# Kernel optimization log

Measured on AMD Instinct MI355X. Metric: run time of the kernel, lower is better.

## Reference

```python
import jax, jax.numpy as jnp
import numpy as np

B, L, D = 2, 2048, 1024
H = 16
HD = D // H
TOP_FRAC = 0.2


def setup_inputs() -> dict:
    key = jax.random.key(0)
    ks = jax.random.split(key, 9)
    s = 1.0 / np.sqrt(D)
    return {
        "x": jax.random.normal(ks[0], (B, L, D), dtype=jnp.float32),
        "Wq": jax.random.normal(ks[1], (D, D), dtype=jnp.float32) * s,
        "bq": jnp.zeros((D,), jnp.float32),
        "Wk": jax.random.normal(ks[2], (D, D), dtype=jnp.float32) * s,
        "bk": jnp.zeros((D,), jnp.float32),
        "Wv": jax.random.normal(ks[3], (D, D), dtype=jnp.float32) * s,
        "bv": jnp.zeros((D,), jnp.float32),
        "Wo": jax.random.normal(ks[4], (D, D), dtype=jnp.float32) * s,
        "bo": jnp.zeros((D,), jnp.float32),
    }


def reference(x, Wq, bq, Wk, bk, Wv, bv, Wo, bo):
    b, l, d = x.shape
    scale = HD ** (-0.5)
    k_top = max(1, int(l * TOP_FRAC))

    def split_heads(t):  # [B,L,D] -> [B,H,L,HD]
        return t.reshape(b, l, H, HD).transpose(0, 2, 1, 3)

    q = split_heads(x @ Wq.T + bq)
    k = split_heads(x @ Wk.T + bk)
    v = split_heads(x @ Wv.T + bv)

    # select top-k queries per (batch, head) by squared L2 norm
    q_norm = jnp.sum(q * q, axis=-1)              # [B,H,L]
    _, topk_idx = jax.lax.top_k(q_norm, k_top)    # [B,H,k_top]
    bi = jnp.arange(b)[:, None, None]
    hi = jnp.arange(H)[None, :, None]
    mask = jnp.zeros((b, H, l), dtype=bool).at[bi, hi, topk_idx].set(True)
    q = q * mask[..., None]                       # zero non-selected queries

    scores = jnp.einsum("bhqd,bhkd->bhqk", q, k) * scale
    probs = jax.nn.softmax(scores, axis=-1)       # zero rows -> uniform 1/L
    out = jnp.einsum("bhqk,bhkd->bhqd", probs, v)
    out = out.transpose(0, 2, 1, 3).reshape(b, l, d)
    return out @ Wo.T + bo
```

## Files before the change

kernel.cpp:

```cpp
#include <hip/hip_runtime.h>
#include <hip/hip_bf16.h>
#include <math.h>

typedef __bf16 bf16_t;
typedef __bf16 bf16x8 __attribute__((ext_vector_type(8)));
typedef __bf16 bf16x4 __attribute__((ext_vector_type(4)));
typedef float  f32x4  __attribute__((ext_vector_type(4)));

#define L_DIM 2048
#define D_DIM 1024
#define H_DIM 16
#define M_DIM 4096
#define KTOP 409
#define SLOTS 512
#define SLOTS_IO 448
#define KSPLIT 8
#define KCHUNK 256
#define HSZ (L_DIM * 64)

__device__ __forceinline__ void split2(float a, bf16_t& h, bf16_t& l) {
  h = (bf16_t)a;
  l = (bf16_t)(a - (float)h);
}

__device__ __forceinline__ void gld16(const bf16_t* g, bf16_t* l) {
  __builtin_amdgcn_global_load_lds(
      (const __attribute__((address_space(1))) void*)g,
      (__attribute__((address_space(3))) void*)l, 16, 0, 0);
}

#define STAGE_TILE128(src, dst)                                               \
  {                                                                           \
    const int seg0 = wave * 2;                                                \
    const int r0 = seg0 * 16 + (lane >> 2);                                   \
    const int c0 = (((lane & 3) ^ ((lane >> 2) & 3))) * 8;                    \
    gld16((src) + (size_t)r0 * D_DIM + c0, (dst) + seg0 * 512);               \
    gld16((src) + (size_t)(r0 + 16) * D_DIM + c0, (dst) + (seg0 + 1) * 512);  \
  }

#define STAGE_TILE64(src, dst)                                                \
  {                                                                           \
    const int r0 = wave * 16 + (lane >> 2);                                   \
    const int c0 = (((lane & 3) ^ ((lane >> 2) & 3))) * 8;                    \
    gld16((src) + (size_t)r0 * D_DIM + c0, (dst) + wave * 512);               \
  }

#define FRAG(buf, ROW) \
  (*reinterpret_cast<const bf16x8*>(&(buf)[(ROW) * 32 + (quad ^ (lm & 3)) * 8]))

__global__ __launch_bounds__(256) void prep_kernel(
    const float* __restrict__ x,  const float* __restrict__ Wq,
    const float* __restrict__ Wk, const float* __restrict__ Wv,
    const float* __restrict__ Wo,
    bf16_t* __restrict__ xhi, bf16_t* __restrict__ xlo,
    bf16_t* __restrict__ Wqhi, bf16_t* __restrict__ Wqlo,
    bf16_t* __restrict__ Wkb,  bf16_t* __restrict__ Wvb,
    bf16_t* __restrict__ Wob,  float* __restrict__ Vmeanf)
{
  const int XV = (M_DIM * D_DIM) / 4;
  const int WV = (D_DIM * D_DIM) / 4;
  const int TOT = XV + 4 * WV + 512;
  for (int i = blockIdx.x * 256 + threadIdx.x; i < TOT; i += gridDim.x * 256) {
    if (i < XV) {
      f32x4 v = ((const f32x4*)x)[i];
      bf16x4 h, l;
      #pragma unroll
      for (int j = 0; j < 4; ++j) { bf16_t hh, ll; split2(v[j], hh, ll); h[j] = hh; l[j] = ll; }
      ((bf16x4*)xhi)[i] = h;
      ((bf16x4*)xlo)[i] = l;
    } else if (i < XV + WV) {
      int j0 = i - XV;
      f32x4 v = ((const f32x4*)Wq)[j0];
      bf16x4 h, l;
      #pragma unroll
      for (int j = 0; j < 4; ++j) { bf16_t hh, ll; split2(v[j], hh, ll); h[j] = hh; l[j] = ll; }
      ((bf16x4*)Wqhi)[j0] = h;
      ((bf16x4*)Wqlo)[j0] = l;
    } else if (i < XV + 2 * WV) {
      int j0 = i - XV - WV;
      f32x4 v = ((const f32x4*)Wk)[j0];
      bf16x4 h;
      #pragma unroll
      for (int j = 0; j < 4; ++j) h[j] = (bf16_t)v[j];
      ((bf16x4*)Wkb)[j0] = h;
    } else if (i < XV + 3 * WV) {
      int j0 = i - XV - 2 * WV;
      f32x4 v = ((const f32x4*)Wv)[j0];
      bf16x4 h;
      #pragma unroll
      for (int j = 0; j < 4; ++j) h[j] = (bf16_t)v[j];
      ((bf16x4*)Wvb)[j0] = h;
    } else if (i < XV + 4 * WV) {
      int j0 = i - XV - 3 * WV;
      f32x4 v = ((const f32x4*)Wo)[j0];
      bf16x4 h;
      #pragma unroll
      for (int j = 0; j < 4; ++j) h[j] = (bf16_t)v[j];
      ((bf16x4*)Wob)[j0] = h;
    } else {
      int j0 = i - XV - 4 * WV;
      f32x4 zz = {0.f, 0.f, 0.f, 0.f};
      ((f32x4*)Vmeanf)[j0] = zz;
    }
  }
}

__global__ __launch_bounds__(256, 3) void gemm_qkv(
    const bf16_t* __restrict__ xhi, const bf16_t* __restrict__ xlo,
    const bf16_t* __restrict__ Wqhi, const bf16_t* __restrict__ Wqlo,
    const bf16_t* __restrict__ Wkb, const bf16_t* __restrict__ Wvb,
    const float* __restrict__ bq, const float* __restrict__ bk, const float* __restrict__ bv,
    bf16_t* __restrict__ Qhi, bf16_t* __restrict__ Khi, bf16_t* __restrict__ VThi,
    float* __restrict__ norms, float* __restrict__ Vmeanf)
{
  const int bx = blockIdx.x;
  const int z  = bx % 3;
  const int id = bx / 3;
  const int n0   = (id & 7) * 128;
  const int row0 = (id >> 3) * 128;

  __shared__ __align__(16) bf16_t sm[2][3][4096];

  const int tid  = threadIdx.x;
  const int lane = tid & 63;
  const int wave = tid >> 6;
  const int wr = wave >> 1, wc = wave & 1;
  const int lm = lane & 15, quad = lane >> 4;

  const f32x4 vzero = {0.f, 0.f, 0.f, 0.f};
  f32x4 acc[4][4];
  #pragma unroll
  for (int mi = 0; mi < 4; ++mi)
    #pragma unroll
    for (int ni = 0; ni < 4; ++ni) acc[mi][ni] = vzero;

  if (z == 0) {
#define STAGE_A(k0, b) do {                                                  \
      STAGE_TILE128(xhi  + (size_t)row0 * D_DIM + (k0), sm[b][0]);           \
      STAGE_TILE128(Wqhi + (size_t)n0   * D_DIM + (k0), sm[b][1]);           \
      STAGE_TILE128(Wqlo + (size_t)n0   * D_DIM + (k0), sm[b][2]);           \
    } while (0)
#define STAGE_B(k0, b) do {                                                  \
      STAGE_TILE128(xlo  + (size_t)row0 * D_DIM + (k0), sm[b][0]);           \
      STAGE_TILE128(Wqhi + (size_t)n0   * D_DIM + (k0), sm[b][1]);           \
    } while (0)

    STAGE_A(0, 0);
    __syncthreads();
    int cur = 0;
    for (int k0 = 0; k0 < D_DIM; k0 += 32) {
      if (k0 + 32 < D_DIM) STAGE_A(k0 + 32, cur ^ 1);
      else                 STAGE_B(0, cur ^ 1);
      bf16x8 af[4], bh0[4], bl0[4];
      #pragma unroll
      for (int mi = 0; mi < 4; ++mi)
        af[mi] = FRAG(sm[cur][0], wr * 64 + mi * 16 + lm);
      #pragma unroll
      for (int ni = 0; ni < 4; ++ni) {
        bh0[ni] = FRAG(sm[cur][1], wc * 64 + ni * 16 + lm);
        bl0[ni] = FRAG(sm[cur][2], wc * 64 + ni * 16 + lm);
      }
      #pragma unroll
      for (int mi = 0; mi < 4; ++mi)
        #pragma unroll
        for (int ni = 0; ni < 4; ++ni) {
          acc[mi][ni] = __builtin_amdgcn_mfma_f32_16x16x32_bf16(af[mi], bh0[ni], acc[mi][ni], 0, 0, 0);
          acc[mi][ni] = __builtin_amdgcn_mfma_f32_16x16x32_bf16(af[mi], bl0[ni], acc[mi][ni], 0, 0, 0);
        }
      __syncthreads();
      cur ^= 1;
    }
    for (int k0 = 0; k0 < D_DIM; k0 += 32) {
      if (k0 + 32 < D_DIM) STAGE_B(k0 + 32, cur ^ 1);
      bf16x8 af[4], bh0[4];
      #pragma unroll
      for (int mi = 0; mi < 4; ++mi)
        af[mi] = FRAG(sm[cur][0], wr * 64 + mi * 16 + lm);
      #pragma unroll
      for (int ni = 0; ni < 4; ++ni)
        bh0[ni] = FRAG(sm[cur][1], wc * 64 + ni * 16 + lm);
      #pragma unroll
      for (int mi = 0; mi < 4; ++mi)
        #pragma unroll
        for (int ni = 0; ni < 4; ++ni)
          acc[mi][ni] = __builtin_amdgcn_mfma_f32_16x16x32_bf16(af[mi], bh0[ni], acc[mi][ni], 0, 0, 0);
      __syncthreads();
      cur ^= 1;
    }

    float bvv[4];
    #pragma unroll
    for (int ni = 0; ni < 4; ++ni) bvv[ni] = bq[n0 + wc * 64 + ni * 16 + lm];
    #pragma unroll
    for (int mi = 0; mi < 4; ++mi)
      #pragma unroll
      for (int ni = 0; ni < 4; ++ni)
        #pragma unroll
        for (int r = 0; r < 4; ++r) acc[mi][ni][r] += bvv[ni];

    const int h = (n0 + wc * 64) >> 6;
    #pragma unroll
    for (int mi = 0; mi < 4; ++mi)
      #pragma unroll
      for (int r = 0; r < 4; ++r) {
        float s = 0.f;
        #pragma unroll
        for (int ni = 0; ni < 4; ++ni) { float v = acc[mi][ni][r]; s += v * v; }
        s += __shfl_xor(s, 1); s += __shfl_xor(s, 2);
        s += __shfl_xor(s, 4); s += __shfl_xor(s, 8);
        if (lm == 0) {
          int row = row0 + wr * 64 + mi * 16 + quad * 4 + r;
          int bb = row >> 11, ll = row & (L_DIM - 1);
          norms[(bb * H_DIM + h) * L_DIM + ll] = s;
        }
      }

    #pragma unroll
    for (int mi = 0; mi < 4; ++mi)
      #pragma unroll
      for (int r = 0; r < 4; ++r) {
        int row = row0 + wr * 64 + mi * 16 + quad * 4 + r;
        #pragma unroll
        for (int ni = 0; ni < 4; ++ni)
          Qhi[(size_t)row * D_DIM + n0 + wc * 64 + ni * 16 + lm] = (bf16_t)acc[mi][ni][r];
      }
  } else {
    const bf16_t* W = (z == 1) ? Wkb : Wvb;
#define STAGE_L(k0, b) do {                                                  \
      STAGE_TILE128(xhi + (size_t)row0 * D_DIM + (k0), sm[b][0]);            \
      STAGE_TILE128(W   + (size_t)n0   * D_DIM + (k0), sm[b][1]);            \
    } while (0)

    STAGE_L(0, 0);
    __syncthreads();
    int cur = 0;
    for (int k0 = 0; k0 < D_DIM; k0 += 32) {
      if (k0 + 32 < D_DIM) STAGE_L(k0 + 32, cur ^ 1);
      bf16x8 af[4], bfr[4];
      #pragma unroll
      for (int mi = 0; mi < 4; ++mi)
        af[mi] = FRAG(sm[cur][0], wr * 64 + mi * 16 + lm);
      #pragma unroll
      for (int ni = 0; ni < 4; ++ni)
        bfr[ni] = FRAG(sm[cur][1], wc * 64 + ni * 16 + lm);
      #pragma unroll
      for (int mi = 0; mi < 4; ++mi)
        #pragma unroll
        for (int ni = 0; ni < 4; ++ni)
          acc[mi][ni] = __builtin_amdgcn_mfma_f32_16x16x32_bf16(af[mi], bfr[ni], acc[mi][ni], 0, 0, 0);
      __syncthreads();
      cur ^= 1;
    }

    const float* bias = (z == 1) ? bk : bv;
    float bvv[4];
    #pragma unroll
    for (int ni = 0; ni < 4; ++ni) bvv[ni] = bias[n0 + wc * 64 + ni * 16 + lm];
    #pragma unroll
    for (int mi = 0; mi < 4; ++mi)
      #pragma unroll
      for (int ni = 0; ni < 4; ++ni)
        #pragma unroll
        for (int r = 0; r < 4; ++r) acc[mi][ni][r] += bvv[ni];

    const int hh = (n0 + wc * 64) >> 6;
    if (z == 1) {
      #pragma unroll
      for (int mi = 0; mi < 4; ++mi)
        #pragma unroll
        for (int r = 0; r < 4; ++r) {
          int row = row0 + wr * 64 + mi * 16 + quad * 4 + r;
          int bb = row >> 11, ll = row & (L_DIM - 1);
          size_t base = (size_t)(bb * H_DIM + hh) * HSZ + (size_t)ll * 64;
          #pragma unroll
          for (int ni = 0; ni < 4; ++ni)
            Khi[base + ni * 16 + lm] = (bf16_t)acc[mi][ni][r];
        }
    } else {
      #pragma unroll
      for (int mi = 0; mi < 4; ++mi) {
        int rbase = row0 + wr * 64 + mi * 16 + quad * 4;
        int bb = rbase >> 11, l0 = rbase & (L_DIM - 1);
        int kbv = l0 >> 5, kin = l0 & 31;
        size_t hb = (size_t)(bb * H_DIM + hh) * HSZ;
        #pragma unroll
        for (int ni = 0; ni < 4; ++ni) {
          int d = ni * 16 + lm;
          bf16x4 wv;
          #pragma unroll
          for (int r = 0; r < 4; ++r) wv[r] = (bf16_t)acc[mi][ni][r];
          *reinterpret_cast<bf16x4*>(&VThi[hb + (size_t)(kbv * 64 + d) * 32 + kin]) = wv;
        }
      }
      const int bb = row0 >> 11;
      float ps[4];
      #pragma unroll
      for (int ni = 0; ni < 4; ++ni) {
        float s = 0.f;
        #pragma unroll
        for (int mi = 0; mi < 4; ++mi)
          #pragma unroll
          for (int r = 0; r < 4; ++r) s += acc[mi][ni][r];
        ps[ni] = s;
      }
      #pragma unroll
      for (int ni = 0; ni < 4; ++ni) {
        ps[ni] += __shfl_xor(ps[ni], 16);
        ps[ni] += __shfl_xor(ps[ni], 32);
      }
      if (quad == 0) {
        #pragma unroll
        for (int ni = 0; ni < 4; ++ni)
          atomicAdd(&Vmeanf[(bb * H_DIM + hh) * 64 + ni * 16 + lm], ps[ni]);
      }
    }
  }
}

__global__ __launch_bounds__(256) void gemm_out(
    const bf16_t* __restrict__ Ahi, const bf16_t* __restrict__ Wob,
    const float* __restrict__ bias, float* __restrict__ C)
{
  const int n0   = blockIdx.x * 128;
  const int row0 = blockIdx.y * 64;

  __shared__ __align__(16) bf16_t sm[2][6144];

  const int tid  = threadIdx.x;
  const int lane = tid & 63;
  const int wave = tid >> 6;
  const int wr = wave >> 1, wc = wave & 1;
  const int lm = lane & 15, quad = lane >> 4;

  const f32x4 vzero = {0.f, 0.f, 0.f, 0.f};
  f32x4 acc[2][4];
  #pragma unroll
  for (int mi = 0; mi < 2; ++mi)
    #pragma unroll
    for (int ni = 0; ni < 4; ++ni) acc[mi][ni] = vzero;

#define STAGE_O(k0, b) do {                                                  \
    STAGE_TILE64(Ahi + (size_t)row0 * D_DIM + (k0), sm[b]);                  \
    STAGE_TILE128(Wob + (size_t)n0 * D_DIM + (k0), sm[b] + 2048);            \
  } while (0)

  STAGE_O(0, 0);
  __syncthreads();
  int cur = 0;
  for (int k0 = 0; k0 < D_DIM; k0 += 32) {
    if (k0 + 32 < D_DIM) STAGE_O(k0 + 32, cur ^ 1);
    bf16x8 af[2], bfr[4];
    #pragma unroll
    for (int mi = 0; mi < 2; ++mi)
      af[mi] = FRAG(sm[cur], wr * 32 + mi * 16 + lm);
    #pragma unroll
    for (int ni = 0; ni < 4; ++ni)
      bfr[ni] = FRAG(sm[cur] + 2048, wc * 64 + ni * 16 + lm);
    #pragma unroll
    for (int mi = 0; mi < 2; ++mi)
      #pragma unroll
      for (int ni = 0; ni < 4; ++ni)
        acc[mi][ni] = __builtin_amdgcn_mfma_f32_16x16x32_bf16(af[mi], bfr[ni], acc[mi][ni], 0, 0, 0);
    __syncthreads();
    cur ^= 1;
  }

  float bvv[4];
  #pragma unroll
  for (int ni = 0; ni < 4; ++ni) bvv[ni] = bias[n0 + wc * 64 + ni * 16 + lm];
  #pragma unroll
  for (int mi = 0; mi < 2; ++mi)
    #pragma unroll
    for (int r = 0; r < 4; ++r) {
      int row = row0 + wr * 32 + mi * 16 + quad * 4 + r;
      #pragma unroll
      for (int ni = 0; ni < 4; ++ni)
        C[(size_t)row * D_DIM + n0 + wc * 64 + ni * 16 + lm] = acc[mi][ni][r] + bvv[ni];
    }
}

__global__ __launch_bounds__(1024) void topk_kernel(
    const float* __restrict__ norms, int* __restrict__ sel,
    int* __restrict__ rowmap)
{
  const int bh = blockIdx.x;
  const int t  = threadIdx.x;
  const int w  = t >> 6;
  const int lane = t & 63;

  __shared__ int bins[256];
  __shared__ unsigned int sh_pfx;
  __shared__ int sh_r;
  __shared__ int cnt0[16], cnt1[16], ecnt0[16], ecnt1[16];

  const unsigned int k0 = __float_as_uint(norms[bh * L_DIM + t]);
  const unsigned int k1 = __float_as_uint(norms[bh * L_DIM + t + 1024]);

  rowmap[bh * L_DIM + t] = -1;
  rowmap[bh * L_DIM + t + 1024] = -1;

  unsigned int pfx = 0;
  int r = KTOP;
  #pragma unroll
  for (int p = 0; p < 4; ++p) {
    const int sh = 24 - 8 * p;
    if (t < 256) bins[t] = 0;
    __syncthreads();
    const bool q0 = (p == 0) || ((k0 >> (sh + 8)) == pfx);
    const bool q1 = (p == 0) || ((k1 >> (sh + 8)) == pfx);
    if (q0) atomicAdd(&bins[(k0 >> sh) & 255], 1);
    if (q1) atomicAdd(&bins[(k1 >> sh) & 255], 1);
    __syncthreads();
    if (w == 0) {
      const int b0 = bins[lane * 4 + 0];
      const int b1 = bins[lane * 4 + 1];
      const int b2 = bins[lane * 4 + 2];
      const int b3 = bins[lane * 4 + 3];
      int sfx = b0 + b1 + b2 + b3;
      #pragma unroll
      for (int off = 1; off < 64; off <<= 1) {
        int other = __shfl_down(sfx, off);
        if (lane + off < 64) sfx += other;
      }
      int nsfx = __shfl_down(sfx, 1);
      if (lane == 63) nsfx = 0;
      if (sfx >= r && nsfx < r) {
        int cum = nsfx, B, rn;
        if (cum + b3 >= r)      { B = lane * 4 + 3; rn = r - cum; }
        else { cum += b3;
          if (cum + b2 >= r)    { B = lane * 4 + 2; rn = r - cum; }
          else { cum += b2;
            if (cum + b1 >= r)  { B = lane * 4 + 1; rn = r - cum; }
            else { cum += b1;     B = lane * 4 + 0; rn = r - cum; }
          }
        }
        sh_pfx = (pfx << 8) | (unsigned int)B;
        sh_r = rn;
      }
    }
    __syncthreads();
    pfx = sh_pfx;
    r = sh_r;
    __syncthreads();
  }
  const unsigned int T = pfx;

  const bool gt0 = (k0 > T), gt1 = (k1 > T);
  const bool eq0 = (k0 == T), eq1 = (k1 == T);
  const unsigned long long mlt = (lane == 63) ? 0x7fffffffffffffffull
                                              : ((1ull << lane) - 1ull);
  const unsigned long long bg0 = __ballot(gt0);
  const unsigned long long bg1 = __ballot(gt1);
  const unsigned long long be0 = __ballot(eq0);
  const unsigned long long be1 = __ballot(eq1);
  if (lane == 0) {
    cnt0[w]  = __popcll(bg0);
    cnt1[w]  = __popcll(bg1);
    ecnt0[w] = __popcll(be0);
    ecnt1[w] = __popcll(be1);
  }
  __syncthreads();
  int og0 = 0, og1 = 0, oe0 = 0, oe1 = 0;
  int tg0 = 0, tg1 = 0, te0 = 0;
  #pragma unroll
  for (int i = 0; i < 16; ++i) {
    if (i < w) { og0 += cnt0[i]; og1 += cnt1[i]; oe0 += ecnt0[i]; oe1 += ecnt1[i]; }
    tg0 += cnt0[i]; tg1 += cnt1[i]; te0 += ecnt0[i];
  }
  const int G = tg0 + tg1;
  const int take = KTOP - G;
  const int base = bh * SLOTS;

  if (gt0) {
    int slot = og0 + __popcll(bg0 & mlt);
    sel[base + slot] = t;
    rowmap[bh * L_DIM + t] = slot;
  }
  if (gt1) {
    int slot = tg0 + og1 + __popcll(bg1 & mlt);
    sel[base + slot] = t + 1024;
    rowmap[bh * L_DIM + t + 1024] = slot;
  }
  if (eq0) {
    int rk = oe0 + __popcll(be0 & mlt);
    if (rk < take) {
      sel[base + G + rk] = t;
      rowmap[bh * L_DIM + t] = G + rk;
    }
  }
  if (eq1) {
    int rk = te0 + oe1 + __popcll(be1 & mlt);
    if (rk < take) {
      sel[base + G + rk] = t + 1024;
      rowmap[bh * L_DIM + t + 1024] = G + rk;
    }
  }
  if (t < SLOTS - KTOP) sel[base + KTOP + t] = -1;
}

__global__ __launch_bounds__(256) void attn_kernel(
    const bf16_t* __restrict__ Qhi,
    const bf16_t* __restrict__ Khi,
    const bf16_t* __restrict__ VThi,
    const int* __restrict__ sel,
    float* __restrict__ Ol, bf16_t* __restrict__ Oo)
{
  const int bx = blockIdx.x;
  const int xl = bx & 7;
  const int rest = bx >> 3;
  const int qc = rest & 3;
  const int gh = rest >> 2;
  const int g  = gh * 8 + xl;
  const int bh = g & 31;
  const int ks = g >> 5;
  const int b = bh >> 4, h = bh & 15;
  const int wave = threadIdx.x >> 6;
  const int lane = threadIdx.x & 63;
  const int lm = lane & 15, quad = lane >> 4;

  __shared__ __align__(16) bf16_t sPh[2][2][4][16][40];

  const int qbase = qc * 128 + wave * 32;
  bf16x8 qa[2][2];
  #pragma unroll
  for (int qt = 0; qt < 2; ++qt) {
    int qi = sel[bh * SLOTS + qbase + qt * 16 + lm];
    size_t qo = ((size_t)(b * L_DIM + (qi >= 0 ? qi : 0))) * D_DIM + h * 64;
    qa[qt][0] = *reinterpret_cast<const bf16x8*>(&Qhi[qo + quad * 8]);
    qa[qt][1] = *reinterpret_cast<const bf16x8*>(&Qhi[qo + 32 + quad * 8]);
  }

  const f32x4 vzero = {0.f, 0.f, 0.f, 0.f};
  float l_l[2][4];
  f32x4 o[2][4];
  #pragma unroll
  for (int qt = 0; qt < 2; ++qt)
    #pragma unroll
    for (int ni = 0; ni < 4; ++ni) { o[qt][ni] = vzero; l_l[qt][ni] = 0.f; }

  const float scale = 0.125f;
  const size_t khead = (size_t)(b * H_DIM + h) * HSZ;
  const int key0 = ks * KCHUNK;

  #pragma unroll 2
  for (int kt = 0; kt < KCHUNK; kt += 32) {
    const int PB = (kt >> 5) & 1;
    size_t kr0 = khead + (size_t)(key0 + kt + lm) * 64;
    size_t kr1 = khead + (size_t)(key0 + kt + 16 + lm) * 64;
    bf16x8 kb0 = *reinterpret_cast<const bf16x8*>(&Khi[kr0 + quad * 8]);
    bf16x8 kb1 = *reinterpret_cast<const bf16x8*>(&Khi[kr0 + 32 + quad * 8]);
    bf16x8 kb2 = *reinterpret_cast<const bf16x8*>(&Khi[kr1 + quad * 8]);
    bf16x8 kb3 = *reinterpret_cast<const bf16x8*>(&Khi[kr1 + 32 + quad * 8]);
    const int kbv = (key0 + kt) >> 5;
    bf16x8 vbh[4];
    #pragma unroll
    for (int ni = 0; ni < 4; ++ni) {
      size_t vo = khead + (size_t)(kbv * 64 + ni * 16 + lm) * 32 + quad * 8;
      vbh[ni] = *reinterpret_cast<const bf16x8*>(&VThi[vo]);
    }
    #pragma unroll
    for (int qt = 0; qt < 2; ++qt) {
      f32x4 s0 = vzero, s1 = vzero;
      s0 = __builtin_amdgcn_mfma_f32_16x16x32_bf16(qa[qt][0], kb0, s0, 0, 0, 0);
      s0 = __builtin_amdgcn_mfma_f32_16x16x32_bf16(qa[qt][1], kb1, s0, 0, 0, 0);
      s1 = __builtin_amdgcn_mfma_f32_16x16x32_bf16(qa[qt][0], kb2, s1, 0, 0, 0);
      s1 = __builtin_amdgcn_mfma_f32_16x16x32_bf16(qa[qt][1], kb3, s1, 0, 0, 0);
      #pragma unroll
      for (int r = 0; r < 4; ++r) {
        float p0 = __expf(s0[r] * scale);
        float p1 = __expf(s1[r] * scale);
        l_l[qt][r] += p0 + p1;
        sPh[PB][qt][wave][quad * 4 + r][lm]      = (bf16_t)p0;
        sPh[PB][qt][wave][quad * 4 + r][16 + lm] = (bf16_t)p1;
      }
      bf16x8 pah = *reinterpret_cast<const bf16x8*>(&sPh[PB][qt][wave][lm][quad * 8]);
      #pragma unroll
      for (int ni = 0; ni < 4; ++ni)
        o[qt][ni] = __builtin_amdgcn_mfma_f32_16x16x32_bf16(pah, vbh[ni], o[qt][ni], 0, 0, 0);
    }
  }

  #pragma unroll
  for (int qt = 0; qt < 2; ++qt)
    #pragma unroll
    for (int r = 0; r < 4; ++r) {
      l_l[qt][r] += __shfl_xor(l_l[qt][r], 1);
      l_l[qt][r] += __shfl_xor(l_l[qt][r], 2);
      l_l[qt][r] += __shfl_xor(l_l[qt][r], 4);
      l_l[qt][r] += __shfl_xor(l_l[qt][r], 8);
    }

  #pragma unroll
  for (int qt = 0; qt < 2; ++qt)
    #pragma unroll
    for (int r = 0; r < 4; ++r) {
      int slot = qbase + qt * 16 + quad * 4 + r;
      int s2 = sel[bh * SLOTS + slot];
      if (s2 >= 0) {
        size_t gs = (size_t)(bh * SLOTS_IO + slot) * KSPLIT + ks;
        if (lm == 0) Ol[gs] = l_l[qt][r];
        #pragma unroll
        for (int ni = 0; ni < 4; ++ni)
          Oo[gs * 64 + ni * 16 + lm] = (bf16_t)o[qt][ni][r];
      }
    }
}

__global__ __launch_bounds__(256) void fill_kernel(
    const float* __restrict__ Ol, const bf16_t* __restrict__ Oo,
    const int* __restrict__ rowmap, const float* __restrict__ Vmeanf,
    bf16_t* __restrict__ AOhi)
{
  const int bh = blockIdx.x;
  const int b = bh >> 4, h = bh & 15;
  const int t = threadIdx.x;
  const int lane = t & 63;
  const int w = t >> 6;

  __shared__ __align__(16) bf16_t smh[64];
  if (t < 64)
    smh[t] = (bf16_t)(Vmeanf[(b * H_DIM + h) * 64 + t] * (1.0f / (float)L_DIM));
  __syncthreads();

  const int rbase = blockIdx.y * 64 + w * 16;
  int flag = -1;
  if (lane < 16) flag = rowmap[bh * L_DIM + rbase + lane];

  for (int j = 0; j < 16; ++j) {
    const int s = __shfl(flag, j);
    const int row = rbase + j;
    bf16_t outv;
    if (s < 0) {
      outv = smh[lane];
    } else {
      size_t gs = (size_t)(bh * SLOTS_IO + s) * KSPLIT;
      float L = 0.f, ov = 0.f;
      #pragma unroll
      for (int sp = 0; sp < KSPLIT; ++sp) {
        L  += Ol[gs + sp];
        ov += (float)Oo[(gs + sp) * 64 + lane];
      }
      outv = (bf16_t)(ov / L);
    }
    AOhi[((size_t)(b * L_DIM + row)) * D_DIM + h * 64 + lane] = outv;
  }
}

extern "C" void kernel_launch(void* const* d_in, const int* in_sizes, int n_in,
                              void* d_out, int out_size, void* d_ws, size_t ws_size,
                              hipStream_t stream) {
  const float* x  = (const float*)d_in[0];
  const float* Wq = (const float*)d_in[1];
  const float* bq = (const float*)d_in[2];
  const float* Wk = (const float*)d_in[3];
  const float* bk = (const float*)d_in[4];
  const float* Wv = (const float*)d_in[5];
  const float* bv = (const float*)d_in[6];
  const float* Wo = (const float*)d_in[7];
  const float* bo = (const float*)d_in[8];
  float* out = (float*)d_out;

  const size_t MB = 1u << 20;
  char* ws = (char*)d_ws;
  bf16_t* Qhi  = (bf16_t*)(ws);
  bf16_t* VThi = (bf16_t*)(ws + 8 * MB);
  bf16_t* xhi  = (bf16_t*)(ws + 16 * MB);
  bf16_t* xlo  = (bf16_t*)(ws + 24 * MB);
  bf16_t* Oo   = (bf16_t*)(ws + 16 * MB);
  int*    rowmap = (int*)(ws + 31 * MB);
  bf16_t* Wqhi = (bf16_t*)(ws + 32 * MB);
  bf16_t* Wqlo = (bf16_t*)(ws + 34 * MB);
  bf16_t* Wkb  = (bf16_t*)(ws + 36 * MB);
  bf16_t* Wvb  = (bf16_t*)(ws + 38 * MB);
  bf16_t* Wob  = (bf16_t*)(ws + 40 * MB);
  float*  norms = (float*)(ws + 42 * MB);
  int*    sel   = (int*)(ws + 42 * MB + (256u << 10));
  float*  Ol    = (float*)(ws + 42 * MB + (320u << 10));
  float*  Vmeanf = (float*)(ws + 42 * MB + (832u << 10));
  bf16_t* AOhi = Qhi;
  bf16_t* Khi = (bf16_t*)d_out;

  dim3 blk(256);
  prep_kernel<<<dim3(2048), blk, 0, stream>>>(x, Wq, Wk, Wv, Wo,
                                              xhi, xlo, Wqhi, Wqlo, Wkb, Wvb, Wob,
                                              Vmeanf);
  gemm_qkv<<<dim3(768), blk, 0, stream>>>(xhi, xlo, Wqhi, Wqlo, Wkb, Wvb,
                                          bq, bk, bv, Qhi, Khi, VThi, norms, Vmeanf);
  topk_kernel<<<dim3(32), dim3(1024), 0, stream>>>(norms, sel, rowmap);
  attn_kernel<<<dim3(32 * 4 * KSPLIT), blk, 0, stream>>>(Qhi, Khi, VThi, sel, Ol, Oo);
  fill_kernel<<<dim3(32, 32), blk, 0, stream>>>(Ol, Oo, rowmap, Vmeanf, AOhi);
  gemm_out<<<dim3(8, 64), blk, 0, stream>>>(AOhi, Wob, bo, out);
}
```

Measured before the change: 214.0 us.

## Stage K/V tiles through double-buffered LDS with XOR swizzle in attention

```diff
diff --git a/kernel.cpp b/kernel.cpp
--- a/kernel.cpp
+++ b/kernel.cpp
@@ -518,6 +518,8 @@
   const int lane = threadIdx.x & 63;
   const int lm = lane & 15, quad = lane >> 4;
 
+  __shared__ __align__(16) bf16_t sK[2][2048];
+  __shared__ __align__(16) bf16_t sV[2][2048];
   __shared__ __align__(16) bf16_t sPh[2][2][4][16][40];
 
   const int qbase = qc * 128 + wave * 32;
@@ -542,21 +544,34 @@
   const size_t khead = (size_t)(b * H_DIM + h) * HSZ;
   const int key0 = ks * KCHUNK;
 
+#define ATTN_STAGE(KT, bsel) do {                                             \
+    const int krow = wave * 8 + (lane >> 3);                                  \
+    const int kslot = (lane & 7) ^ ((lane >> 3) & 7);                         \
+    gld16(&Khi[khead + (size_t)(key0 + (KT) + krow) * 64 + kslot * 8],        \
+          sK[bsel] + wave * 512);                                             \
+    const int vrow = wave * 16 + (lane >> 2);                                 \
+    const int vslot = (lane & 3) ^ ((lane >> 2) & 3);                         \
+    const size_t vbase = khead + (size_t)((key0 + (KT)) >> 5) * 2048;         \
+    gld16(&VThi[vbase + vrow * 32 + vslot * 8], sV[bsel] + wave * 512);       \
+  } while (0)
+
+  ATTN_STAGE(0, 0);
+  __syncthreads();
+  int cur = 0;
   #pragma unroll 2
   for (int kt = 0; kt < KCHUNK; kt += 32) {
+    if (kt + 32 < KCHUNK) ATTN_STAGE(kt + 32, cur ^ 1);
     const int PB = (kt >> 5) & 1;
-    size_t kr0 = khead + (size_t)(key0 + kt + lm) * 64;
-    size_t kr1 = khead + (size_t)(key0 + kt + 16 + lm) * 64;
-    bf16x8 kb0 = *reinterpret_cast<const bf16x8*>(&Khi[kr0 + quad * 8]);
-    bf16x8 kb1 = *reinterpret_cast<const bf16x8*>(&Khi[kr0 + 32 + quad * 8]);
-    bf16x8 kb2 = *reinterpret_cast<const bf16x8*>(&Khi[kr1 + quad * 8]);
-    bf16x8 kb3 = *reinterpret_cast<const bf16x8*>(&Khi[kr1 + 32 + quad * 8]);
-    const int kbv = (key0 + kt) >> 5;
+    const int kx = lm & 7;
+    bf16x8 kb0 = *reinterpret_cast<const bf16x8*>(&sK[cur][lm * 64 + ((quad) ^ kx) * 8]);
+    bf16x8 kb1 = *reinterpret_cast<const bf16x8*>(&sK[cur][lm * 64 + ((quad + 4) ^ kx) * 8]);
+    bf16x8 kb2 = *reinterpret_cast<const bf16x8*>(&sK[cur][(16 + lm) * 64 + ((quad) ^ kx) * 8]);
+    bf16x8 kb3 = *reinterpret_cast<const bf16x8*>(&sK[cur][(16 + lm) * 64 + ((quad + 4) ^ kx) * 8]);
     bf16x8 vbh[4];
     #pragma unroll
     for (int ni = 0; ni < 4; ++ni) {
-      size_t vo = khead + (size_t)(kbv * 64 + ni * 16 + lm) * 32 + quad * 8;
-      vbh[ni] = *reinterpret_cast<const bf16x8*>(&VThi[vo]);
+      const int vr = ni * 16 + lm;
+      vbh[ni] = *reinterpret_cast<const bf16x8*>(&sV[cur][vr * 32 + ((quad) ^ (vr & 3)) * 8]);
     }
     #pragma unroll
     for (int qt = 0; qt < 2; ++qt) {
@@ -578,6 +593,8 @@
       for (int ni = 0; ni < 4; ++ni)
         o[qt][ni] = __builtin_amdgcn_mfma_f32_16x16x32_bf16(pah, vbh[ni], o[qt][ni], 0, 0, 0);
     }
+    __syncthreads();
+    cur ^= 1;
   }
 
   #pragma unroll
```

Measured after the change: 200.5 us (median of 2 runs). 6.3% less time.
